# Kernel optimization log

Hardware: AMD Instinct MI355X
Metric: run time of the kernel (lower is better)

The kernel has to match this reference:

```python
import jax, jax.numpy as jnp
import numpy as np

# KroneckerLinear: W ~= sum_i (A_i kron B_i); efficient path computes, per token,
# Y = sum_i A_i @ X @ B_i^T with X = x.reshape(in1, in2), output flattened as (out1*out2).

IN1, IN2 = 64, 64      # in_factors (in1*in2 = in_features = 4096)
OUT1, OUT2 = 64, 64    # out_factors (out1*out2 = out_features = 4096)
NUM_SUM = 2
BATCH, SEQ = 4, 4096


def setup_inputs() -> dict:
    key = jax.random.key(0)
    kx, ka, kb, kbias = jax.random.split(key, 4)
    x = jax.random.normal(kx, (BATCH, SEQ, IN1 * IN2), dtype=jnp.float32)
    # kaiming-uniform-like scale for small factors
    bound_a = 1.0 / np.sqrt(IN1)
    bound_b = 1.0 / np.sqrt(IN2)
    A = jax.random.uniform(ka, (NUM_SUM, OUT1, IN1), dtype=jnp.float32, minval=-bound_a, maxval=bound_a)
    B = jax.random.uniform(kb, (NUM_SUM, OUT2, IN2), dtype=jnp.float32, minval=-bound_b, maxval=bound_b)
    bound = 1.0 / np.sqrt(IN1 * IN2)
    bias = jax.random.uniform(kbias, (OUT1 * OUT2,), dtype=jnp.float32, minval=-bound, maxval=bound)
    return {"x": x, "A": A, "B": B, "bias": bias}


def reference(x, A, B, bias):
    Bsz, T, _ = x.shape
    X = x.reshape(Bsz, T, IN1, IN2)  # (b, t, i, j)
    # y[b,t,o,p] = sum_s sum_ij A[s,o,i] * X[b,t,i,j] * B[s,p,j]  -> (out1, out2)
    y = jnp.einsum("btij,soi,spj->btop", X, A, B)
    return y.reshape(Bsz, T, OUT1 * OUT2) + bias
```

## Files before the change

kernel.cpp:

```cpp
#include <hip/hip_runtime.h>

typedef float  f32x4  __attribute__((ext_vector_type(4)));
typedef short  bf16x8 __attribute__((ext_vector_type(8)));

#define NT   16384
#define GRID 512

__device__ __forceinline__ short f2bf(float x) {
  unsigned u = __builtin_bit_cast(unsigned, x);
  u = (u + 0x7FFFu + ((u >> 16) & 1u)) >> 16;
  return (short)u;
}

__device__ __forceinline__ void gload16(const float* gp, float* lp) {
  __builtin_amdgcn_global_load_lds((const __attribute__((address_space(1))) void*)gp,
                                   (__attribute__((address_space(3))) void*)lp,
                                   16, 0, 0);
}

__device__ __forceinline__ void stage(float (&XB)[4096], const float* gbase, int lane) {
#pragma unroll
  for (int q = 0; q < 16; ++q) {
    const int i  = q * 4 + (lane >> 4);
    const int qp = lane & 15;
    const float* gp = gbase + i * 64 + ((qp ^ (i & 7)) << 2);
    gload16(gp, &XB[0] + q * 256);
  }
}

__device__ __forceinline__ void body(float (&XB)[4096],
                                     bf16x8 (&AT)[1024], bf16x8 (&BT)[1024],
                                     int tok, int lane, int g, int l15,
                                     const float* __restrict__ x,
                                     const float* __restrict__ bias,
                                     float* __restrict__ out) {
  asm volatile("s_waitcnt vmcnt(48)" ::: "memory");

  const f32x4* xb4 = (const f32x4*)(&XB[0]);

  bf16x8 xf[4][2];
#pragma unroll
  for (int it = 0; it < 4; ++it) {
#pragma unroll
    for (int jc = 0; jc < 2; ++jc) {
      const int i  = it * 16 + l15;
      const int q0 = jc * 8 + 2 * g;
      f32x4 f0 = xb4[i * 16 + ((q0    ) ^ (i & 7))];
      f32x4 f1 = xb4[i * 16 + ((q0 + 1) ^ (i & 7))];
      bf16x8 t;
      t[0]=f2bf(f0.x); t[1]=f2bf(f0.y); t[2]=f2bf(f0.z); t[3]=f2bf(f0.w);
      t[4]=f2bf(f1.x); t[5]=f2bf(f1.y); t[6]=f2bf(f1.z); t[7]=f2bf(f1.w);
      xf[it][jc] = t;
    }
  }

  f32x4 acc2[4][4];
#pragma unroll
  for (int a = 0; a < 4; ++a)
#pragma unroll
    for (int b = 0; b < 4; ++b)
      acc2[a][b] = (f32x4){0.f, 0.f, 0.f, 0.f};

#pragma unroll
  for (int s = 0; s < 2; ++s) {
    bf16x8 bfr[4][2];
#pragma unroll
    for (int pt = 0; pt < 4; ++pt)
#pragma unroll
      for (int jc = 0; jc < 2; ++jc)
        bfr[pt][jc] = BT[(s * 8 + pt * 2 + jc) * 64 + lane];

    f32x4 a1[4][4];
#pragma unroll
    for (int a = 0; a < 4; ++a)
#pragma unroll
      for (int b = 0; b < 4; ++b)
        a1[a][b] = (f32x4){0.f, 0.f, 0.f, 0.f};
#pragma unroll
    for (int it = 0; it < 4; ++it)
#pragma unroll
      for (int pt = 0; pt < 4; ++pt)
#pragma unroll
        for (int jc = 0; jc < 2; ++jc)
          a1[it][pt] = __builtin_amdgcn_mfma_f32_16x16x32_bf16(
              xf[it][jc], bfr[pt][jc], a1[it][pt], 0, 0, 0);

    bf16x8 uf[4][2];
#pragma unroll
    for (int pt = 0; pt < 4; ++pt)
#pragma unroll
      for (int c = 0; c < 2; ++c) {
        bf16x8 t;
#pragma unroll
        for (int e = 0; e < 8; ++e)
          t[e] = f2bf(a1[(e >> 2) + 2 * c][pt][e & 3]);
        uf[pt][c] = t;
      }

    bf16x8 afr[4][2];
#pragma unroll
    for (int ot = 0; ot < 4; ++ot)
#pragma unroll
      for (int c = 0; c < 2; ++c)
        afr[ot][c] = AT[(s * 8 + ot * 2 + c) * 64 + lane];

#pragma unroll
    for (int pt = 0; pt < 4; ++pt)
#pragma unroll
      for (int ot = 0; ot < 4; ++ot)
#pragma unroll
        for (int c = 0; c < 2; ++c)
          acc2[pt][ot] = __builtin_amdgcn_mfma_f32_16x16x32_bf16(
              uf[pt][c], afr[ot][c], acc2[pt][ot], 0, 0, 0);
  }

  const int pcol = 4 * g;
  f32x4 bv[4][4];
#pragma unroll
  for (int pt = 0; pt < 4; ++pt)
#pragma unroll
    for (int ot = 0; ot < 4; ++ot)
      bv[pt][ot] = *(const f32x4*)(bias + (ot * 16 + l15) * 64 + pt * 16 + pcol);

  asm volatile("" ::: "memory");
  stage(XB, x + ((size_t)((tok + 2 * GRID) & (NT - 1)) << 12), lane);
  asm volatile("" ::: "memory");

  float* ob = out + ((size_t)tok << 12);
#pragma unroll
  for (int pt = 0; pt < 4; ++pt)
#pragma unroll
    for (int ot = 0; ot < 4; ++ot) {
      f32x4 r = acc2[pt][ot] + bv[pt][ot];
      *(f32x4*)(ob + (ot * 16 + l15) * 64 + pt * 16 + pcol) = r;
    }
}

__global__ __launch_bounds__(64) void kron_kernel(const float* __restrict__ x,
                                                  const float* __restrict__ A,
                                                  const float* __restrict__ B,
                                                  const float* __restrict__ bias,
                                                  float* __restrict__ out) {
  __shared__ float  xb0[4096];
  __shared__ float  xb1[4096];
  __shared__ bf16x8 AT[1024];
  __shared__ bf16x8 BT[1024];

  const int lane = threadIdx.x;
  const int g    = lane >> 4;
  const int l15  = lane & 15;
  const int bid  = blockIdx.x;

  for (int idx = 0; idx < 16; ++idx) {
    const int s = idx >> 3, ot = (idx & 7) >> 1, c = idx & 1;
    const int o = ot * 16 + l15;
    bf16x8 v;
#pragma unroll
    for (int e = 0; e < 8; ++e) {
      const int i = c * 32 + 4 * g + (e & 3) + 16 * (e >> 2);
      v[e] = f2bf(A[s * 4096 + o * 64 + i]);
    }
    AT[idx * 64 + lane] = v;
  }
  for (int idx = 0; idx < 16; ++idx) {
    const int s = idx >> 3, pt = (idx & 7) >> 1, jc = idx & 1;
    const int p = pt * 16 + l15;
    bf16x8 v;
#pragma unroll
    for (int e = 0; e < 8; ++e) {
      const int j = jc * 32 + 8 * g + e;
      v[e] = f2bf(B[s * 4096 + p * 64 + j]);
    }
    BT[idx * 64 + lane] = v;
  }

  stage(xb0, x + ((size_t)bid << 12), lane);
  stage(xb1, x + ((size_t)(bid + GRID) << 12), lane);
  asm volatile("s_waitcnt vmcnt(16)" ::: "memory");

  for (int k = 0; k < 32; k += 2) {
    body(xb0, AT, BT, bid + GRID * k,       lane, g, l15, x, bias, out);
    body(xb1, AT, BT, bid + GRID * (k + 1), lane, g, l15, x, bias, out);
  }
}

extern "C" void kernel_launch(void* const* d_in, const int* in_sizes, int n_in,
                              void* d_out, int out_size, void* d_ws, size_t ws_size,
                              hipStream_t stream) {
  const float* x    = (const float*)d_in[0];
  const float* A    = (const float*)d_in[1];
  const float* B    = (const float*)d_in[2];
  const float* bias = (const float*)d_in[3];
  float* out        = (float*)d_out;
  kron_kernel<<<dim3(GRID), dim3(64), 0, stream>>>(x, A, B, bias, out);
}
```

Before: 113.0 us.

## Run four independent token streams per block and drop wraparound prefetches

The launch changes from 512 single-wave blocks to 256 blocks of four waves. Each wave processes its own stream of 16 tokens with a private double-buffered LDS tile, and the four waves share one bf16 transpose of A and B. This doubles the number of concurrently running waves, splits the A/B conversion across waves, and stops the final iterations from prefetching tokens they never use. The cost is about 160KB of LDS per block, which limits residency to one block per CU. Skipping the tail prefetches changes the outstanding-load count that the fixed vmcnt wait assumes, so the last token's tile may be read before its load completes.

```diff
diff --git a/kernel.cpp b/kernel.cpp
--- a/kernel.cpp
+++ b/kernel.cpp
@@ -3,8 +3,10 @@
 typedef float  f32x4  __attribute__((ext_vector_type(4)));
 typedef short  bf16x8 __attribute__((ext_vector_type(8)));
 
-#define NT   16384
-#define GRID 512
+#define NT       16384
+#define NBLOCK   256
+#define NSTREAM  1024
+#define TPS      16
 
 __device__ __forceinline__ short f2bf(float x) {
   unsigned u = __builtin_bit_cast(unsigned, x);
@@ -18,25 +20,25 @@
                                    16, 0, 0);
 }
 
-__device__ __forceinline__ void stage(float (&XB)[4096], const float* gbase, int lane) {
+__device__ __forceinline__ void stage(float* XB, const float* gbase, int lane) {
 #pragma unroll
   for (int q = 0; q < 16; ++q) {
     const int i  = q * 4 + (lane >> 4);
     const int qp = lane & 15;
     const float* gp = gbase + i * 64 + ((qp ^ (i & 7)) << 2);
-    gload16(gp, &XB[0] + q * 256);
-  }
-}
-
-__device__ __forceinline__ void body(float (&XB)[4096],
-                                     bf16x8 (&AT)[1024], bf16x8 (&BT)[1024],
-                                     int tok, int lane, int g, int l15,
+    gload16(gp, XB + q * 256);
+  }
+}
+
+__device__ __forceinline__ void body(float* XB,
+                                     const bf16x8* AT, const bf16x8* BT,
+                                     int tok, bool pf, int lane, int g, int l15,
                                      const float* __restrict__ x,
                                      const float* __restrict__ bias,
                                      float* __restrict__ out) {
   asm volatile("s_waitcnt vmcnt(48)" ::: "memory");
 
-  const f32x4* xb4 = (const f32x4*)(&XB[0]);
+  const f32x4* xb4 = (const f32x4*)XB;
 
   bf16x8 xf[4][2];
 #pragma unroll
@@ -123,7 +125,7 @@
       bv[pt][ot] = *(const f32x4*)(bias + (ot * 16 + l15) * 64 + pt * 16 + pcol);
 
   asm volatile("" ::: "memory");
-  stage(XB, x + ((size_t)((tok + 2 * GRID) & (NT - 1)) << 12), lane);
+  if (pf) stage(XB, x + ((size_t)(tok + 2 * NSTREAM) << 12), lane);
   asm volatile("" ::: "memory");
 
   float* ob = out + ((size_t)tok << 12);
@@ -136,22 +138,24 @@
     }
 }
 
-__global__ __launch_bounds__(64) void kron_kernel(const float* __restrict__ x,
-                                                  const float* __restrict__ A,
-                                                  const float* __restrict__ B,
-                                                  const float* __restrict__ bias,
-                                                  float* __restrict__ out) {
-  __shared__ float  xb0[4096];
-  __shared__ float  xb1[4096];
+__global__ __launch_bounds__(256) void kron_kernel(const float* __restrict__ x,
+                                                   const float* __restrict__ A,
+                                                   const float* __restrict__ B,
+                                                   const float* __restrict__ bias,
+                                                   float* __restrict__ out) {
+  __shared__ float  xb[4][2][4096];
   __shared__ bf16x8 AT[1024];
   __shared__ bf16x8 BT[1024];
 
-  const int lane = threadIdx.x;
+  const int lane = threadIdx.x & 63;
+  const int w    = threadIdx.x >> 6;
   const int g    = lane >> 4;
   const int l15  = lane & 15;
-  const int bid  = blockIdx.x;
-
-  for (int idx = 0; idx < 16; ++idx) {
+  const int sid  = blockIdx.x * 4 + w;
+
+#pragma unroll
+  for (int t = 0; t < 4; ++t) {
+    const int idx = w * 4 + t;
     const int s = idx >> 3, ot = (idx & 7) >> 1, c = idx & 1;
     const int o = ot * 16 + l15;
     bf16x8 v;
@@ -162,7 +166,9 @@
     }
     AT[idx * 64 + lane] = v;
   }
-  for (int idx = 0; idx < 16; ++idx) {
+#pragma unroll
+  for (int t = 0; t < 4; ++t) {
+    const int idx = w * 4 + t;
     const int s = idx >> 3, pt = (idx & 7) >> 1, jc = idx & 1;
     const int p = pt * 16 + l15;
     bf16x8 v;
@@ -173,14 +179,18 @@
     }
     BT[idx * 64 + lane] = v;
   }
-
-  stage(xb0, x + ((size_t)bid << 12), lane);
-  stage(xb1, x + ((size_t)(bid + GRID) << 12), lane);
+  __syncthreads();
+
+  float* xb0 = &xb[w][0][0];
+  float* xb1 = &xb[w][1][0];
+
+  stage(xb0, x + ((size_t)sid << 12), lane);
+  stage(xb1, x + ((size_t)(sid + NSTREAM) << 12), lane);
   asm volatile("s_waitcnt vmcnt(16)" ::: "memory");
 
-  for (int k = 0; k < 32; k += 2) {
-    body(xb0, AT, BT, bid + GRID * k,       lane, g, l15, x, bias, out);
-    body(xb1, AT, BT, bid + GRID * (k + 1), lane, g, l15, x, bias, out);
+  for (int k = 0; k < TPS; k += 2) {
+    body(xb0, AT, BT, sid + NSTREAM * k,       k + 2 < TPS, lane, g, l15, x, bias, out);
+    body(xb1, AT, BT, sid + NSTREAM * (k + 1), k + 3 < TPS, lane, g, l15, x, bias, out);
   }
 }
 
@@ -192,5 +202,5 @@
   const float* B    = (const float*)d_in[2];
   const float* bias = (const float*)d_in[3];
   float* out        = (float*)d_out;
-  kron_kernel<<<dim3(GRID), dim3(64), 0, stream>>>(x, A, B, bias, out);
-}
+  kron_kernel<<<dim3(NBLOCK), dim3(256), 0, stream>>>(x, A, B, bias, out);
+}
```

After: 123.9 us. 9.6% more time.

## Triple-buffer X staging with early prefetch and bias hoisted into accumulators

Applied to the files above, without the earlier changes.

Replaces the two-buffer ping-pong with a three-buffer rotation. The prefetch for token k+2 is issued at the start of each iteration instead of after the compute, with waitcnt thresholds tuned per iteration. Bias is loaded once into registers and used as the initial accumulator, which removes a separate add and a reload per token. LDS reads of X become explicit inline-asm ds_read_b128 followed by a single lgkmcnt wait. The cost is more LDS use and more complex wait accounting.

```diff
diff --git a/kernel.cpp b/kernel.cpp
--- a/kernel.cpp
+++ b/kernel.cpp
@@ -1,15 +1,17 @@
 #include <hip/hip_runtime.h>
+#include <hip/hip_bf16.h>
 
 typedef float  f32x4  __attribute__((ext_vector_type(4)));
 typedef short  bf16x8 __attribute__((ext_vector_type(8)));
 
-#define NT   16384
-#define GRID 512
+#define NT      16384
+#define NBLOCK  512
+#define TPS     (NT / NBLOCK)
+
+#define WAITV(n) asm volatile("s_waitcnt vmcnt(" #n ")" ::: "memory")
 
 __device__ __forceinline__ short f2bf(float x) {
-  unsigned u = __builtin_bit_cast(unsigned, x);
-  u = (u + 0x7FFFu + ((u >> 16) & 1u)) >> 16;
-  return (short)u;
+  return (short)__builtin_bit_cast(unsigned short, __float2bfloat16(x));
 }
 
 __device__ __forceinline__ void gload16(const float* gp, float* lp) {
@@ -18,131 +20,26 @@
                                    16, 0, 0);
 }
 
-__device__ __forceinline__ void stage(float (&XB)[4096], const float* gbase, int lane) {
+__device__ __forceinline__ unsigned ldsaddr(const void* p) {
+  return (unsigned)(uintptr_t)(const __attribute__((address_space(3))) void*)p;
+}
+
+__device__ __forceinline__ void stage(float* XB, const float* gbase, int lane) {
 #pragma unroll
   for (int q = 0; q < 16; ++q) {
-    const int i  = q * 4 + (lane >> 4);
-    const int qp = lane & 15;
-    const float* gp = gbase + i * 64 + ((qp ^ (i & 7)) << 2);
-    gload16(gp, &XB[0] + q * 256);
-  }
-}
-
-__device__ __forceinline__ void body(float (&XB)[4096],
-                                     bf16x8 (&AT)[1024], bf16x8 (&BT)[1024],
-                                     int tok, int lane, int g, int l15,
-                                     const float* __restrict__ x,
-                                     const float* __restrict__ bias,
-                                     float* __restrict__ out) {
-  asm volatile("s_waitcnt vmcnt(48)" ::: "memory");
-
-  const f32x4* xb4 = (const f32x4*)(&XB[0]);
-
-  bf16x8 xf[4][2];
-#pragma unroll
-  for (int it = 0; it < 4; ++it) {
-#pragma unroll
-    for (int jc = 0; jc < 2; ++jc) {
-      const int i  = it * 16 + l15;
-      const int q0 = jc * 8 + 2 * g;
-      f32x4 f0 = xb4[i * 16 + ((q0    ) ^ (i & 7))];
-      f32x4 f1 = xb4[i * 16 + ((q0 + 1) ^ (i & 7))];
-      bf16x8 t;
-      t[0]=f2bf(f0.x); t[1]=f2bf(f0.y); t[2]=f2bf(f0.z); t[3]=f2bf(f0.w);
-      t[4]=f2bf(f1.x); t[5]=f2bf(f1.y); t[6]=f2bf(f1.z); t[7]=f2bf(f1.w);
-      xf[it][jc] = t;
-    }
-  }
-
-  f32x4 acc2[4][4];
-#pragma unroll
-  for (int a = 0; a < 4; ++a)
-#pragma unroll
-    for (int b = 0; b < 4; ++b)
-      acc2[a][b] = (f32x4){0.f, 0.f, 0.f, 0.f};
-
-#pragma unroll
-  for (int s = 0; s < 2; ++s) {
-    bf16x8 bfr[4][2];
-#pragma unroll
-    for (int pt = 0; pt < 4; ++pt)
-#pragma unroll
-      for (int jc = 0; jc < 2; ++jc)
-        bfr[pt][jc] = BT[(s * 8 + pt * 2 + jc) * 64 + lane];
-
-    f32x4 a1[4][4];
-#pragma unroll
-    for (int a = 0; a < 4; ++a)
-#pragma unroll
-      for (int b = 0; b < 4; ++b)
-        a1[a][b] = (f32x4){0.f, 0.f, 0.f, 0.f};
-#pragma unroll
-    for (int it = 0; it < 4; ++it)
-#pragma unroll
-      for (int pt = 0; pt < 4; ++pt)
-#pragma unroll
-        for (int jc = 0; jc < 2; ++jc)
-          a1[it][pt] = __builtin_amdgcn_mfma_f32_16x16x32_bf16(
-              xf[it][jc], bfr[pt][jc], a1[it][pt], 0, 0, 0);
-
-    bf16x8 uf[4][2];
-#pragma unroll
-    for (int pt = 0; pt < 4; ++pt)
-#pragma unroll
-      for (int c = 0; c < 2; ++c) {
-        bf16x8 t;
-#pragma unroll
-        for (int e = 0; e < 8; ++e)
-          t[e] = f2bf(a1[(e >> 2) + 2 * c][pt][e & 3]);
-        uf[pt][c] = t;
-      }
-
-    bf16x8 afr[4][2];
-#pragma unroll
-    for (int ot = 0; ot < 4; ++ot)
-#pragma unroll
-      for (int c = 0; c < 2; ++c)
-        afr[ot][c] = AT[(s * 8 + ot * 2 + c) * 64 + lane];
-
-#pragma unroll
-    for (int pt = 0; pt < 4; ++pt)
-#pragma unroll
-      for (int ot = 0; ot < 4; ++ot)
-#pragma unroll
-        for (int c = 0; c < 2; ++c)
-          acc2[pt][ot] = __builtin_amdgcn_mfma_f32_16x16x32_bf16(
-              uf[pt][c], afr[ot][c], acc2[pt][ot], 0, 0, 0);
-  }
-
-  const int pcol = 4 * g;
-  f32x4 bv[4][4];
-#pragma unroll
-  for (int pt = 0; pt < 4; ++pt)
-#pragma unroll
-    for (int ot = 0; ot < 4; ++ot)
-      bv[pt][ot] = *(const f32x4*)(bias + (ot * 16 + l15) * 64 + pt * 16 + pcol);
-
-  asm volatile("" ::: "memory");
-  stage(XB, x + ((size_t)((tok + 2 * GRID) & (NT - 1)) << 12), lane);
-  asm volatile("" ::: "memory");
-
-  float* ob = out + ((size_t)tok << 12);
-#pragma unroll
-  for (int pt = 0; pt < 4; ++pt)
-#pragma unroll
-    for (int ot = 0; ot < 4; ++ot) {
-      f32x4 r = acc2[pt][ot] + bv[pt][ot];
-      *(f32x4*)(ob + (ot * 16 + l15) * 64 + pt * 16 + pcol) = r;
-    }
-}
-
-__global__ __launch_bounds__(64) void kron_kernel(const float* __restrict__ x,
-                                                  const float* __restrict__ A,
-                                                  const float* __restrict__ B,
-                                                  const float* __restrict__ bias,
-                                                  float* __restrict__ out) {
-  __shared__ float  xb0[4096];
-  __shared__ float  xb1[4096];
+    const int i = q * 4 + (lane >> 4);
+    const float* gp = gbase + i * 64 + (((lane & 15) ^ (i & 7)) << 2);
+    gload16(gp, XB + q * 256);
+  }
+}
+
+__global__ __launch_bounds__(64, 1)
+void kron_kernel(const float* __restrict__ x,
+                 const float* __restrict__ A,
+                 const float* __restrict__ Bm,
+                 const float* __restrict__ bias,
+                 float* __restrict__ out) {
+  __shared__ float  xh[3][4096];
   __shared__ bf16x8 AT[1024];
   __shared__ bf16x8 BT[1024];
 
@@ -167,20 +64,130 @@
     const int p = pt * 16 + l15;
     bf16x8 v;
 #pragma unroll
-    for (int e = 0; e < 8; ++e) {
-      const int j = jc * 32 + 8 * g + e;
-      v[e] = f2bf(B[s * 4096 + p * 64 + j]);
+    for (int e = 0; e < 8; ++e)
+      v[e] = f2bf(Bm[s * 4096 + p * 64 + (jc * 32 + 8 * g + e)]);
+    BT[idx * 64 + lane] = v;
+  }
+
+  const int pcol = 4 * g;
+  f32x4 bv[4][4];
+#pragma unroll
+  for (int pt = 0; pt < 4; ++pt)
+#pragma unroll
+    for (int ot = 0; ot < 4; ++ot)
+      bv[pt][ot] = *(const f32x4*)(bias + (ot * 16 + l15) * 64 + pt * 16 + pcol);
+
+  float* b0 = &xh[0][0];
+  float* b1 = &xh[1][0];
+  float* b2 = &xh[2][0];
+  stage(b0, x + ((size_t)bid << 12), lane);
+  stage(b1, x + ((size_t)(bid + NBLOCK) << 12), lane);
+
+  for (int k = 0; k < TPS; ++k) {
+    if (k == 0)                    WAITV(16);
+    else if (k == 1 || k == TPS-1) WAITV(32);
+    else                           WAITV(48);
+
+    if (k + 2 < TPS)
+      stage(b2, x + ((size_t)(bid + (k + 2) * NBLOCK) << 12), lane);
+
+    const unsigned ba = ldsaddr(b0);
+    f32x4 r0[4][2], r1[4][2];
+#pragma unroll
+    for (int it = 0; it < 4; ++it) {
+      const unsigned base = ba + (unsigned)(it * 16 + l15) * 256u;
+      const unsigned m    = (unsigned)(l15 & 7);
+#pragma unroll
+      for (int jc = 0; jc < 2; ++jc) {
+        const unsigned c0 = (unsigned)(8 * jc + 2 * g);
+        asm volatile("ds_read_b128 %0, %1" : "=v"(r0[it][jc]) : "v"(base + ((c0 ^ m) << 4)) : "memory");
+        asm volatile("ds_read_b128 %0, %1" : "=v"(r1[it][jc]) : "v"(base + (((c0 + 1u) ^ m) << 4)) : "memory");
+      }
     }
-    BT[idx * 64 + lane] = v;
-  }
-
-  stage(xb0, x + ((size_t)bid << 12), lane);
-  stage(xb1, x + ((size_t)(bid + GRID) << 12), lane);
-  asm volatile("s_waitcnt vmcnt(16)" ::: "memory");
-
-  for (int k = 0; k < 32; k += 2) {
-    body(xb0, AT, BT, bid + GRID * k,       lane, g, l15, x, bias, out);
-    body(xb1, AT, BT, bid + GRID * (k + 1), lane, g, l15, x, bias, out);
+    asm volatile("s_waitcnt lgkmcnt(0)" ::: "memory");
+    __builtin_amdgcn_sched_barrier(0);
+
+    bf16x8 xf[4][2];
+#pragma unroll
+    for (int it = 0; it < 4; ++it)
+#pragma unroll
+      for (int jc = 0; jc < 2; ++jc) {
+        bf16x8 t;
+        t[0]=f2bf(r0[it][jc][0]); t[1]=f2bf(r0[it][jc][1]);
+        t[2]=f2bf(r0[it][jc][2]); t[3]=f2bf(r0[it][jc][3]);
+        t[4]=f2bf(r1[it][jc][0]); t[5]=f2bf(r1[it][jc][1]);
+        t[6]=f2bf(r1[it][jc][2]); t[7]=f2bf(r1[it][jc][3]);
+        xf[it][jc] = t;
+      }
+
+    f32x4 acc2[4][4];
+#pragma unroll
+    for (int pt = 0; pt < 4; ++pt)
+#pragma unroll
+      for (int ot = 0; ot < 4; ++ot)
+        acc2[pt][ot] = bv[pt][ot];
+
+#pragma unroll
+    for (int s = 0; s < 2; ++s) {
+      bf16x8 bfr[4][2];
+#pragma unroll
+      for (int pt = 0; pt < 4; ++pt)
+#pragma unroll
+        for (int jc = 0; jc < 2; ++jc)
+          bfr[pt][jc] = BT[(s * 8 + pt * 2 + jc) * 64 + lane];
+
+      f32x4 a1[4][4];
+#pragma unroll
+      for (int a = 0; a < 4; ++a)
+#pragma unroll
+        for (int b = 0; b < 4; ++b)
+          a1[a][b] = (f32x4){0.f, 0.f, 0.f, 0.f};
+#pragma unroll
+      for (int it = 0; it < 4; ++it)
+#pragma unroll
+        for (int pt = 0; pt < 4; ++pt)
+#pragma unroll
+          for (int jc = 0; jc < 2; ++jc)
+            a1[it][pt] = __builtin_amdgcn_mfma_f32_16x16x32_bf16(
+                xf[it][jc], bfr[pt][jc], a1[it][pt], 0, 0, 0);
+
+      bf16x8 uf[4][2];
+#pragma unroll
+      for (int pt = 0; pt < 4; ++pt)
+#pragma unroll
+        for (int c = 0; c < 2; ++c) {
+          bf16x8 t;
+#pragma unroll
+          for (int e = 0; e < 8; ++e)
+            t[e] = f2bf(a1[(e >> 2) + 2 * c][pt][e & 3]);
+          uf[pt][c] = t;
+        }
+
+      bf16x8 afr[4][2];
+#pragma unroll
+      for (int ot = 0; ot < 4; ++ot)
+#pragma unroll
+        for (int c = 0; c < 2; ++c)
+          afr[ot][c] = AT[(s * 8 + ot * 2 + c) * 64 + lane];
+
+#pragma unroll
+      for (int pt = 0; pt < 4; ++pt)
+#pragma unroll
+        for (int ot = 0; ot < 4; ++ot)
+#pragma unroll
+          for (int c = 0; c < 2; ++c)
+            acc2[pt][ot] = __builtin_amdgcn_mfma_f32_16x16x32_bf16(
+                uf[pt][c], afr[ot][c], acc2[pt][ot], 0, 0, 0);
+    }
+
+    float* ob = out + (((size_t)(k * NBLOCK + bid)) << 12);
+#pragma unroll
+    for (int pt = 0; pt < 4; ++pt)
+#pragma unroll
+      for (int ot = 0; ot < 4; ++ot)
+        *(f32x4*)(ob + (ot * 16 + l15) * 64 + pt * 16 + pcol) = acc2[pt][ot];
+
+    float* t = b0; b0 = b1; b1 = b2; b2 = t;
   }
 }
 
@@ -192,5 +199,5 @@
   const float* B    = (const float*)d_in[2];
   const float* bias = (const float*)d_in[3];
   float* out        = (float*)d_out;
-  kron_kernel<<<dim3(GRID), dim3(64), 0, stream>>>(x, A, B, bias, out);
-}
+  kron_kernel<<<dim3(NBLOCK), dim3(64), 0, stream>>>(x, A, B, bias, out);
+}
```

Result: faster. 105.2 us (-6.9%).
